# Optimization experiments

Hardware: AMD Instinct MI355X
Metric: run time of the kernel (lower is better)

## Reference

```python
import jax, jax.numpy as jnp
import numpy as np

N = 50000       # nodes
E = 800000      # edges (before self-loops)
IN = 64         # in_channels
OUT = 64        # out_channels


def setup_inputs() -> dict:
    key = jax.random.key(0)
    ks = jax.random.split(key, 6)
    X = jax.random.normal(ks[0], (N, IN), jnp.float32)
    H = jax.random.normal(ks[1], (N, OUT), jnp.float32)
    edge_index = jax.random.randint(ks[2], (2, E), 0, N, dtype=jnp.int64)
    edge_weight = jax.random.uniform(ks[3], (E,), jnp.float32)
    fan_in = IN + OUT
    W1 = jax.random.normal(ks[4], (fan_in, 2 * OUT), jnp.float32) / np.sqrt(fan_in).astype(np.float32)
    b1 = jnp.ones((2 * OUT,), jnp.float32)   # TGCN sets graph_conv1.bias to ones
    W2 = jax.random.normal(ks[5], (fan_in, OUT), jnp.float32) / np.sqrt(fan_in).astype(np.float32)
    b2 = jnp.zeros((OUT,), jnp.float32)      # default GCNConv bias init
    return {"X": X, "H": H, "edge_index": edge_index, "edge_weight": edge_weight,
            "W1": W1, "b1": b1, "W2": W2, "b2": b2}


def _gcn_conv(x, W, b, src, dst, w, n):
    """PyG GCNConv: linear transform, add self-loops (fill=1, improved=False),
    symmetric deg^-1/2 normalization, scatter-add aggregation at dst, + bias."""
    x = x @ W                                   # [N, out]
    loop = jnp.arange(n, dtype=src.dtype)
    s = jnp.concatenate([src, loop])            # [E+N]
    d = jnp.concatenate([dst, loop])
    ww = jnp.concatenate([w, jnp.ones((n,), x.dtype)])
    deg = jax.ops.segment_sum(ww, d, num_segments=n)
    dinv = jnp.where(deg > 0, jax.lax.rsqrt(jnp.maximum(deg, 1e-12)), 0.0)
    norm = dinv[s] * ww * dinv[d]               # [E+N]
    msg = x[s] * norm[:, None]                  # gather + scale
    out = jax.ops.segment_sum(msg, d, num_segments=n)  # scatter-add at dst
    return out + b


def reference(X, H, edge_index, edge_weight, W1, b1, W2, b2):
    src, dst = edge_index[0], edge_index[1]
    n = X.shape[0]
    ru = jax.nn.sigmoid(_gcn_conv(jnp.concatenate([X, H], axis=1), W1, b1, src, dst, edge_weight, n))
    r, u = ru[:, :OUT], ru[:, OUT:]             # chunk into reset/update gates
    c = jnp.tanh(_gcn_conv(jnp.concatenate([X, H * r], axis=1), W2, b2, src, dst, edge_weight, n))
    return u * H + (1.0 - u) * c                # new hidden state [N, OUT]
```

## Files before the change

### kernel.cpp

```cpp
#include <hip/hip_runtime.h>
#include <hip/hip_bf16.h>
#include <hip/hip_fp16.h>

#define NN 50000
#define NE 800000
#define NBIN ((NN + 255) / 256)
#define PB ((NE + 1023) / 1024)
#define GB ((NN + 63) / 64)
#define MAXB 4864

typedef __attribute__((ext_vector_type(8))) short bf16x8;
typedef __attribute__((ext_vector_type(4))) float f32x4;
typedef __attribute__((ext_vector_type(2))) float f32x2;

__device__ __forceinline__ unsigned int f2bf(float x) {
    unsigned int u = __float_as_uint(x);
    return (u + 0x7FFFu + ((u >> 16) & 1u)) >> 16;
}
__device__ __forceinline__ float bf2f(unsigned int b) {
    return __uint_as_float(b << 16);
}
__device__ __forceinline__ float4 f8x4_dec(unsigned int u) {
    f32x2 lo = __builtin_amdgcn_cvt_pk_f32_fp8(u, false);
    f32x2 hi = __builtin_amdgcn_cvt_pk_f32_fp8(u, true);
    float4 r; r.x = lo[0]; r.y = lo[1]; r.z = hi[0]; r.w = hi[1];
    return r;
}

__global__ void k_wprep(const float* __restrict__ W1, const float* __restrict__ W2,
                        unsigned short* __restrict__ Wf1,
                        unsigned short* __restrict__ Wf2t,
                        unsigned short* __restrict__ Wf2b) {
    int i = blockIdx.x * 256 + threadIdx.x;
    if (i < 16384) {
        int j = i & 7, l = (i >> 3) & 63, n = (i >> 9) & 7, kc = i >> 12;
        int k = kc * 32 + ((l >> 4) << 3) + j;
        int col = (n << 4) + (l & 15);
        Wf1[i] = (unsigned short)f2bf(W1[k * 128 + col]);
    }
    if (i < 4096) {
        int j = i & 7, l = (i >> 3) & 63, n = (i >> 9) & 3, kc = i >> 11;
        int k = kc * 32 + ((l >> 4) << 3) + j;
        int col = (n << 4) + (l & 15);
        Wf2t[i] = (unsigned short)f2bf(W2[k * 64 + col]);
        Wf2b[i] = (unsigned short)f2bf(W2[(k + 64) * 64 + col]);
    }
}

template <int OUTC, int KC, int SRC, int OMODE>
__device__ __forceinline__ void mgemm_core(
    const float* __restrict__ X, const float* __restrict__ Hm,
    const unsigned int* __restrict__ RUb, const unsigned short* __restrict__ Wf,
    const float* __restrict__ addF,
    unsigned short* __restrict__ outH, float* __restrict__ outF,
    unsigned char* __restrict__ outF8,
    int bid, unsigned short* aS, unsigned short* wS)
{
    constexpr int NT = OUTC / 16;
    const int tid = threadIdx.x;
    const int row0 = bid * 64;

    constexpr int WH = KC * NT * 64 * 8;
    {
        const uint4* Wg4 = reinterpret_cast<const uint4*>(Wf);
        uint4* wS4 = reinterpret_cast<uint4*>(wS);
        #pragma unroll
        for (int i = tid; i < WH / 8; i += 256) wS4[i] = Wg4[i];
    }
    #pragma unroll
    for (int i = tid; i < 64 * KC * 8; i += 256) {
        int row = i / (KC * 8), f4 = i % (KC * 8);
        int g = row0 + row;
        float4 v = {0.f, 0.f, 0.f, 0.f};
        if (g < NN) {
            if (SRC == 0) {
                v = (f4 < 16) ? reinterpret_cast<const float4*>(X)[g * 16 + f4]
                              : reinterpret_cast<const float4*>(Hm)[g * 16 + f4 - 16];
            } else if (SRC == 1) {
                v = reinterpret_cast<const float4*>(X)[g * 16 + f4];
            } else {
                v = reinterpret_cast<const float4*>(Hm)[g * 16 + f4];
                unsigned int r0 = RUb[g * 64 + 2 * f4];
                unsigned int r1 = RUb[g * 64 + 2 * f4 + 1];
                v.x *= bf2f(r0 & 0xFFFFu); v.y *= bf2f(r0 >> 16);
                v.z *= bf2f(r1 & 0xFFFFu); v.w *= bf2f(r1 >> 16);
            }
        }
        int k = f4 * 4;
        int kc = k >> 5, ko = k & 31;
        int l = (row & 15) | ((ko >> 3) << 4);
        int j0 = ko & 7;
        int m = row >> 4;
        uint2 pk;
        pk.x = f2bf(v.x) | (f2bf(v.y) << 16);
        pk.y = f2bf(v.z) | (f2bf(v.w) << 16);
        *reinterpret_cast<uint2*>(aS + (((m * KC + kc) * 64 + l) * 8 + j0)) = pk;
    }
    __syncthreads();

    const int wid = tid >> 6, l = tid & 63;
    f32x4 acc[NT];
    #pragma unroll
    for (int n = 0; n < NT; ++n) acc[n] = {0.f, 0.f, 0.f, 0.f};

    const bf16x8* aF = reinterpret_cast<const bf16x8*>(aS);
    const bf16x8* wF = reinterpret_cast<const bf16x8*>(wS);
    #pragma unroll
    for (int kc = 0; kc < KC; ++kc) {
        bf16x8 a = aF[(wid * KC + kc) * 64 + l];
        #pragma unroll
        for (int n = 0; n < NT; ++n) {
            bf16x8 b = wF[(kc * NT + n) * 64 + l];
            acc[n] = __builtin_amdgcn_mfma_f32_16x16x32_bf16(a, b, acc[n], 0, 0, 0);
        }
    }

    const int rbase = row0 + wid * 16 + ((l >> 4) << 2);
    const int cl = l & 15;
    #pragma unroll
    for (int n = 0; n < NT; ++n) {
        #pragma unroll
        for (int i = 0; i < 4; ++i) {
            int row = rbase + i;
            if (row >= NN) continue;
            int col = n * 16 + cl;
            if (OMODE == 1) {
                outF[(size_t)row * OUTC + col] = acc[n][i];
            } else if (OMODE == 2) {
                float a2 = acc[n][i] + addF[(size_t)row * OUTC + col];
                outH[(size_t)row * OUTC + col] = (unsigned short)f2bf(a2);
            } else {
                int q = __builtin_amdgcn_cvt_pk_fp8_f32(acc[n][i], acc[n][i], 0, false);
                outF8[(size_t)row * OUTC + col] = (unsigned char)(q & 0xFF);
            }
        }
    }
}

__launch_bounds__(256)
__global__ void k_build(const float* __restrict__ X, const float* __restrict__ Hm,
                        const unsigned short* __restrict__ Wf1,
                        const unsigned short* __restrict__ Wf2t,
                        unsigned char* __restrict__ Zf8, float* __restrict__ Z2p,
                        const int* __restrict__ dst, int* __restrict__ HT) {
    __shared__ unsigned short aS[8192];
    __shared__ unsigned short wS[16384];
    const int bid = blockIdx.x;
    const int tid = threadIdx.x;
    if (bid < PB) {
        int* hist = reinterpret_cast<int*>(aS);
        for (int i = tid; i < NBIN; i += 256) hist[i] = 0;
        __syncthreads();
        const int base = bid * 1024 + tid;
        #pragma unroll
        for (int k = 0; k < 4; ++k) {
            int e = base + k * 256;
            if (e < NE) atomicAdd(&hist[dst[e] >> 8], 1);
        }
        __syncthreads();
        for (int i = tid; i < NBIN; i += 256) HT[i * PB + bid] = hist[i];
        return;
    }
    if (bid < PB + GB) {
        mgemm_core<128, 4, 0, 3>(X, Hm, nullptr, Wf1, nullptr,
                                 nullptr, nullptr, Zf8, bid - PB, aS, wS);
        return;
    }
    mgemm_core<64, 2, 1, 1>(X, Hm, nullptr, Wf2t, nullptr,
                            nullptr, Z2p, nullptr, bid - PB - GB, aS, wS);
}

__launch_bounds__(256)
__global__ void k_gemm2b(const float* __restrict__ X, const float* __restrict__ Hm,
                         const unsigned int* __restrict__ RUb,
                         const unsigned short* __restrict__ Wf2b,
                         const float* __restrict__ Z2p,
                         unsigned short* __restrict__ Z2b) {
    __shared__ unsigned short aS[4096];
    __shared__ unsigned short wS[4096];
    mgemm_core<64, 2, 2, 2>(X, Hm, RUb, Wf2b, Z2p, Z2b, nullptr, nullptr,
                            blockIdx.x, aS, wS);
}

__launch_bounds__(256)
__global__ void k_scanA1(const int* __restrict__ HT, int* __restrict__ within,
                         int* __restrict__ binTot) {
    __shared__ int lds[PB];
    __shared__ int sc[256];
    __shared__ int carryS;
    const int b = blockIdx.x, tid = threadIdx.x;
    if (tid == 0) carryS = 0;
    for (int i = tid; i < PB; i += 256) lds[i] = HT[b * PB + i];
    __syncthreads();
    for (int c0 = 0; c0 < PB; c0 += 256) {
        int i = c0 + tid;
        int v = (i < PB) ? lds[i] : 0;
        sc[tid] = v;
        __syncthreads();
        #pragma unroll
        for (int off = 1; off < 256; off <<= 1) {
            int t = (tid >= off) ? sc[tid - off] : 0;
            __syncthreads();
            sc[tid] += t;
            __syncthreads();
        }
        int carry = carryS;
        if (i < PB) lds[i] = carry + sc[tid] - v;
        __syncthreads();
        if (tid == 255) carryS = carry + sc[255];
        __syncthreads();
    }
    for (int i = tid; i < PB; i += 256) within[b * PB + i] = lds[i];
    if (tid == 0) binTot[b] = carryS;
}

__launch_bounds__(256)
__global__ void k_scatterA(const int* __restrict__ src, const int* __restrict__ dst,
                           const float* __restrict__ w, const int* __restrict__ binTot,
                           const int* __restrict__ within, uint2* __restrict__ rec) {
    __shared__ int bS[256];
    __shared__ int cur[NBIN];
    const int blk = blockIdx.x, tid = threadIdx.x;
    int bv = (tid < NBIN) ? binTot[tid] : 0;
    bS[tid] = bv;
    __syncthreads();
    #pragma unroll
    for (int off = 1; off < 256; off <<= 1) {
        int t = (tid >= off) ? bS[tid - off] : 0;
        __syncthreads();
        bS[tid] += t;
        __syncthreads();
    }
    if (tid < NBIN) cur[tid] = (bS[tid] - bv) + within[tid * PB + blk];
    __syncthreads();
    const int base = blk * 1024 + tid;
    #pragma unroll
    for (int k = 0; k < 4; ++k) {
        int e = base + k * 256;
        if (e < NE) {
            int d = dst[e];
            int pos = atomicAdd(&cur[d >> 8], 1);
            unsigned int hn = __half_as_ushort(__float2half(w[e]));
            uint2 r;
            r.x = (unsigned int)src[e] | (hn << 16);
            r.y = (unsigned int)d;
            rec[pos] = r;
        }
    }
}

__launch_bounds__(256)
__global__ void k_phase2(const uint2* __restrict__ rec, const int* __restrict__ binTot,
                         unsigned int* __restrict__ snP, int* __restrict__ start,
                         float* __restrict__ dinv) {
    __shared__ unsigned int rSn[MAXB];
    __shared__ unsigned char rLo[MAXB];
    __shared__ unsigned int outSn[MAXB];
    __shared__ int cnt[256];
    __shared__ int sc[256];
    __shared__ int lstart[256];
    __shared__ int cur[256];
    const int b = blockIdx.x, tid = threadIdx.x;

    int bv = (tid < NBIN) ? binTot[tid] : 0;
    sc[tid] = bv;
    __syncthreads();
    #pragma unroll
    for (int off = 1; off < 256; off <<= 1) {
        int t = (tid >= off) ? sc[tid - off] : 0;
        __syncthreads();
        sc[tid] += t;
        __syncthreads();
    }
    const int e0 = (b == 0) ? 0 : sc[b - 1];
    int nE = sc[b] - e0;
    __syncthreads();
    if (nE > MAXB) nE = MAXB;

    cnt[tid] = 0;
    __syncthreads();
    for (int i = tid; i < nE; i += 256) {
        uint2 r = rec[e0 + i];
        rSn[i] = r.x;
        int lo = r.y & 255;
        rLo[i] = (unsigned char)lo;
        atomicAdd(&cnt[lo], 1);
    }
    __syncthreads();
    sc[tid] = cnt[tid];
    __syncthreads();
    #pragma unroll
    for (int off = 1; off < 256; off <<= 1) {
        int t = (tid >= off) ? sc[tid - off] : 0;
        __syncthreads();
        sc[tid] += t;
        __syncthreads();
    }
    lstart[tid] = sc[tid] - cnt[tid];
    cur[tid] = sc[tid] - cnt[tid];
    __syncthreads();
    const int node = b * 256 + tid;
    if (node <= NN) start[node] = e0 + lstart[tid];
    for (int i = tid; i < nE; i += 256) {
        int p = atomicAdd(&cur[rLo[i]], 1);
        outSn[p] = rSn[i];
    }
    __syncthreads();
    for (int i = tid; i < nE; i += 256) snP[e0 + i] = outSn[i];
    {
        int s0 = lstart[tid], c = cnt[tid];
        float sum = 0.f;
        for (int i = s0; i < s0 + c; ++i)
            sum += __half2float(__ushort_as_half((unsigned short)(outSn[i] >> 16)));
        if (node < NN) dinv[node] = rsqrtf(1.0f + sum);
    }
}

__launch_bounds__(256)
__global__ void k_gather1(const int* __restrict__ start, const unsigned int* __restrict__ snP,
                          const unsigned int* __restrict__ Zf8, const float* __restrict__ dinv,
                          const float* __restrict__ bias, uint2* __restrict__ RUb2) {
    const int node = blockIdx.x * 8 + (threadIdx.x >> 5);
    const int l = threadIdx.x & 31;
    if (node >= NN) return;

    const int e0 = start[node], e1 = start[node + 1];
    const float dvd = dinv[node];
    float4 acc = f8x4_dec(Zf8[(size_t)node * 32 + l]);
    acc.x *= dvd; acc.y *= dvd; acc.z *= dvd; acc.w *= dvd;

    #define EFMA8(U, NM) { float4 zz = f8x4_dec(U); \
        acc.x += zz.x * (NM); acc.y += zz.y * (NM); \
        acc.z += zz.z * (NM); acc.w += zz.w * (NM); }
    #define NMOF(SN) (dinv[(SN) & 0xFFFFu] * \
        __half2float(__ushort_as_half((unsigned short)((SN) >> 16))))

    int e = e0;
    for (; e + 8 <= e1; e += 8) {
        unsigned sn0 = snP[e],     sn1 = snP[e + 1], sn2 = snP[e + 2], sn3 = snP[e + 3];
        unsigned sn4 = snP[e + 4], sn5 = snP[e + 5], sn6 = snP[e + 6], sn7 = snP[e + 7];
        unsigned z0 = Zf8[(size_t)(sn0 & 0xFFFFu) * 32 + l];
        unsigned z1 = Zf8[(size_t)(sn1 & 0xFFFFu) * 32 + l];
        unsigned z2 = Zf8[(size_t)(sn2 & 0xFFFFu) * 32 + l];
        unsigned z3 = Zf8[(size_t)(sn3 & 0xFFFFu) * 32 + l];
        unsigned z4 = Zf8[(size_t)(sn4 & 0xFFFFu) * 32 + l];
        unsigned z5 = Zf8[(size_t)(sn5 & 0xFFFFu) * 32 + l];
        unsigned z6 = Zf8[(size_t)(sn6 & 0xFFFFu) * 32 + l];
        unsigned z7 = Zf8[(size_t)(sn7 & 0xFFFFu) * 32 + l];
        float n0 = NMOF(sn0), n1 = NMOF(sn1), n2 = NMOF(sn2), n3 = NMOF(sn3);
        float n4 = NMOF(sn4), n5 = NMOF(sn5), n6 = NMOF(sn6), n7 = NMOF(sn7);
        EFMA8(z0, n0) EFMA8(z1, n1) EFMA8(z2, n2) EFMA8(z3, n3)
        EFMA8(z4, n4) EFMA8(z5, n5) EFMA8(z6, n6) EFMA8(z7, n7)
    }
    if (e + 4 <= e1) {
        unsigned sn0 = snP[e], sn1 = snP[e + 1], sn2 = snP[e + 2], sn3 = snP[e + 3];
        unsigned z0 = Zf8[(size_t)(sn0 & 0xFFFFu) * 32 + l];
        unsigned z1 = Zf8[(size_t)(sn1 & 0xFFFFu) * 32 + l];
        unsigned z2 = Zf8[(size_t)(sn2 & 0xFFFFu) * 32 + l];
        unsigned z3 = Zf8[(size_t)(sn3 & 0xFFFFu) * 32 + l];
        float n0 = NMOF(sn0), n1 = NMOF(sn1), n2 = NMOF(sn2), n3 = NMOF(sn3);
        EFMA8(z0, n0) EFMA8(z1, n1) EFMA8(z2, n2) EFMA8(z3, n3)
        e += 4;
    }
    for (; e < e1; ++e) {
        unsigned sn = snP[e];
        unsigned z = Zf8[(size_t)(sn & 0xFFFFu) * 32 + l];
        float nm = NMOF(sn);
        EFMA8(z, nm)
    }
    #undef EFMA8
    #undef NMOF

    const int c = l * 4;
    float4 bb = *reinterpret_cast<const float4*>(bias + c);
    acc.x = acc.x * dvd + bb.x; acc.y = acc.y * dvd + bb.y;
    acc.z = acc.z * dvd + bb.z; acc.w = acc.w * dvd + bb.w;

    float4 o;
    o.x = 1.f / (1.f + expf(-acc.x));
    o.y = 1.f / (1.f + expf(-acc.y));
    o.z = 1.f / (1.f + expf(-acc.z));
    o.w = 1.f / (1.f + expf(-acc.w));
    uint2 pk;
    pk.x = f2bf(o.x) | (f2bf(o.y) << 16);
    pk.y = f2bf(o.z) | (f2bf(o.w) << 16);
    RUb2[(size_t)node * 32 + l] = pk;
}

__launch_bounds__(256)
__global__ void k_gather2(const int* __restrict__ start, const unsigned int* __restrict__ snP,
                          const uint2* __restrict__ Zb, const float* __restrict__ dinv,
                          const float* __restrict__ bias, const uint2* __restrict__ RUb2,
                          const float* __restrict__ Hm, float* __restrict__ out) {
    constexpr int GRP = 16;
    const int node = blockIdx.x * 16 + threadIdx.x / GRP;
    const int l = threadIdx.x % GRP;
    if (node >= NN) return;

    const int e0 = start[node], e1 = start[node + 1];
    const float dvd = dinv[node];

    uint2 zs = Zb[(size_t)node * GRP + l];
    float4 acc;
    acc.x = bf2f(zs.x & 0xFFFFu) * dvd;
    acc.y = bf2f(zs.x >> 16) * dvd;
    acc.z = bf2f(zs.y & 0xFFFFu) * dvd;
    acc.w = bf2f(zs.y >> 16) * dvd;

    #define EFMA(Z, NM) \
        acc.x += bf2f((Z).x & 0xFFFFu) * (NM); \
        acc.y += bf2f((Z).x >> 16) * (NM);     \
        acc.z += bf2f((Z).y & 0xFFFFu) * (NM); \
        acc.w += bf2f((Z).y >> 16) * (NM);
    #define NMOF(SN) (dinv[(SN) & 0xFFFFu] * \
        __half2float(__ushort_as_half((unsigned short)((SN) >> 16))))

    int e = e0;
    for (; e + 8 <= e1; e += 8) {
        unsigned sn0 = snP[e],     sn1 = snP[e + 1], sn2 = snP[e + 2], sn3 = snP[e + 3];
        unsigned sn4 = snP[e + 4], sn5 = snP[e + 5], sn6 = snP[e + 6], sn7 = snP[e + 7];
        uint2 z0 = Zb[(size_t)(sn0 & 0xFFFFu) * GRP + l];
        uint2 z1 = Zb[(size_t)(sn1 & 0xFFFFu) * GRP + l];
        uint2 z2 = Zb[(size_t)(sn2 & 0xFFFFu) * GRP + l];
        uint2 z3 = Zb[(size_t)(sn3 & 0xFFFFu) * GRP + l];
        uint2 z4 = Zb[(size_t)(sn4 & 0xFFFFu) * GRP + l];
        uint2 z5 = Zb[(size_t)(sn5 & 0xFFFFu) * GRP + l];
        uint2 z6 = Zb[(size_t)(sn6 & 0xFFFFu) * GRP + l];
        uint2 z7 = Zb[(size_t)(sn7 & 0xFFFFu) * GRP + l];
        float n0 = NMOF(sn0), n1 = NMOF(sn1), n2 = NMOF(sn2), n3 = NMOF(sn3);
        float n4 = NMOF(sn4), n5 = NMOF(sn5), n6 = NMOF(sn6), n7 = NMOF(sn7);
        EFMA(z0, n0) EFMA(z1, n1) EFMA(z2, n2) EFMA(z3, n3)
        EFMA(z4, n4) EFMA(z5, n5) EFMA(z6, n6) EFMA(z7, n7)
    }
    if (e + 4 <= e1) {
        unsigned sn0 = snP[e], sn1 = snP[e + 1], sn2 = snP[e + 2], sn3 = snP[e + 3];
        uint2 z0 = Zb[(size_t)(sn0 & 0xFFFFu) * GRP + l];
        uint2 z1 = Zb[(size_t)(sn1 & 0xFFFFu) * GRP + l];
        uint2 z2 = Zb[(size_t)(sn2 & 0xFFFFu) * GRP + l];
        uint2 z3 = Zb[(size_t)(sn3 & 0xFFFFu) * GRP + l];
        float n0 = NMOF(sn0), n1 = NMOF(sn1), n2 = NMOF(sn2), n3 = NMOF(sn3);
        EFMA(z0, n0) EFMA(z1, n1) EFMA(z2, n2) EFMA(z3, n3)
        e += 4;
    }
    for (; e < e1; ++e) {
        unsigned sn = snP[e];
        uint2 z = Zb[(size_t)(sn & 0xFFFFu) * GRP + l];
        float nm = NMOF(sn);
        EFMA(z, nm)
    }
    #undef EFMA
    #undef NMOF

    const int c = l * 4;
    float4 bb = *reinterpret_cast<const float4*>(bias + c);
    acc.x = acc.x * dvd + bb.x; acc.y = acc.y * dvd + bb.y;
    acc.z = acc.z * dvd + bb.z; acc.w = acc.w * dvd + bb.w;

    uint2 uu = RUb2[(size_t)node * 32 + 16 + l];
    float u0 = bf2f(uu.x & 0xFFFFu), u1 = bf2f(uu.x >> 16);
    float u2 = bf2f(uu.y & 0xFFFFu), u3 = bf2f(uu.y >> 16);
    float4 h4 = *reinterpret_cast<const float4*>(Hm + (size_t)node * 64 + c);
    float4 o;
    o.x = u0 * h4.x + (1.f - u0) * tanhf(acc.x);
    o.y = u1 * h4.y + (1.f - u1) * tanhf(acc.y);
    o.z = u2 * h4.z + (1.f - u2) * tanhf(acc.z);
    o.w = u3 * h4.w + (1.f - u3) * tanhf(acc.w);
    *reinterpret_cast<float4*>(out + (size_t)node * 64 + c) = o;
}

extern "C" void kernel_launch(void* const* d_in, const int* in_sizes, int n_in,
                              void* d_out, int out_size, void* d_ws, size_t ws_size,
                              hipStream_t stream) {
    const float* X  = (const float*)d_in[0];
    const float* Hm = (const float*)d_in[1];
    const int*   ei = (const int*)d_in[2];
    const float* w  = (const float*)d_in[3];
    const float* W1 = (const float*)d_in[4];
    const float* b1 = (const float*)d_in[5];
    const float* W2 = (const float*)d_in[6];
    const float* b2 = (const float*)d_in[7];
    float* out = (float*)d_out;

    const int* src = ei;
    const int* dst = ei + NE;

    char* p = (char*)d_ws;
    uint2* rec   = (uint2*)p;  p += sizeof(uint2) * NE;
    uint2* Z2b   = (uint2*)p;  p += sizeof(uint2) * NN * 16;
    uint2* RUb2  = (uint2*)p;  p += sizeof(uint2) * NN * 32;
    float* Z2p   = (float*)p;  p += sizeof(float) * NN * 64;
    float* dinv  = (float*)p;  p += sizeof(float) * NN;
    int*   start = (int*)p;    p += sizeof(int) * (NN + 1);
    int*   binTot   = (int*)p; p += sizeof(int) * (NBIN + 1);
    int*   HT       = (int*)p; p += sizeof(int) * NBIN * PB;
    int*   within   = (int*)p; p += sizeof(int) * NBIN * PB;
    unsigned int* snP = (unsigned int*)p; p += sizeof(unsigned int) * NE;
    unsigned int* Zf8 = (unsigned int*)p; p += sizeof(unsigned int) * NN * 32;
    unsigned short* Wf1  = (unsigned short*)p; p += sizeof(unsigned short) * 16384;
    unsigned short* Wf2t = (unsigned short*)p; p += sizeof(unsigned short) * 4096;
    unsigned short* Wf2b = (unsigned short*)p; p += sizeof(unsigned short) * 4096;

    k_wprep<<<64, 256, 0, stream>>>(W1, W2, Wf1, Wf2t, Wf2b);

    k_build<<<PB + 2 * GB, 256, 0, stream>>>(X, Hm, Wf1, Wf2t,
                                             (unsigned char*)Zf8, Z2p, dst, HT);

    k_scanA1<<<NBIN, 256, 0, stream>>>(HT, within, binTot);
    k_scatterA<<<PB, 256, 0, stream>>>(src, dst, w, binTot, within, rec);
    k_phase2<<<NBIN, 256, 0, stream>>>(rec, binTot, snP, start, dinv);

    k_gather1<<<(NN + 7) / 8, 256, 0, stream>>>(start, snP, Zf8, dinv, b1, RUb2);

    k_gemm2b<<<GB, 256, 0, stream>>>(X, Hm, (const unsigned int*)RUb2, Wf2b, Z2p,
                                     (unsigned short*)Z2b);
    k_gather2<<<(NN + 15) / 16, 256, 0, stream>>>(start, snP, Z2b, dinv, b2, RUb2, Hm, out);
}
```

Before: 114.7 us.

## Fuse reset-gated H·W2 GEMM into first gather kernel

Removes the separate k_gemm2b launch. The first gather kernel now computes (H*r)·W2_bottom per node with fp32 FMAs from LDS-resident weights, adds Z2p, and writes Z2b directly. It keeps only the update gate as bf16 for the second gather. This saves a launch and the round trip of the r gate through global memory. In exchange the gather becomes a persistent grid-stride kernel with block-wide syncs, LDS weights and scalar FMA instead of MFMA, which may reduce latency hiding in the gather.

```diff
diff --git a/kernel.cpp b/kernel.cpp
--- a/kernel.cpp
+++ b/kernel.cpp
@@ -29,8 +29,7 @@
 
 __global__ void k_wprep(const float* __restrict__ W1, const float* __restrict__ W2,
                         unsigned short* __restrict__ Wf1,
-                        unsigned short* __restrict__ Wf2t,
-                        unsigned short* __restrict__ Wf2b) {
+                        unsigned short* __restrict__ Wf2t) {
     int i = blockIdx.x * 256 + threadIdx.x;
     if (i < 16384) {
         int j = i & 7, l = (i >> 3) & 63, n = (i >> 9) & 7, kc = i >> 12;
@@ -43,17 +42,14 @@
         int k = kc * 32 + ((l >> 4) << 3) + j;
         int col = (n << 4) + (l & 15);
         Wf2t[i] = (unsigned short)f2bf(W2[k * 64 + col]);
-        Wf2b[i] = (unsigned short)f2bf(W2[(k + 64) * 64 + col]);
     }
 }
 
 template <int OUTC, int KC, int SRC, int OMODE>
 __device__ __forceinline__ void mgemm_core(
     const float* __restrict__ X, const float* __restrict__ Hm,
-    const unsigned int* __restrict__ RUb, const unsigned short* __restrict__ Wf,
-    const float* __restrict__ addF,
-    unsigned short* __restrict__ outH, float* __restrict__ outF,
-    unsigned char* __restrict__ outF8,
+    const unsigned short* __restrict__ Wf,
+    float* __restrict__ outF, unsigned char* __restrict__ outF8,
     int bid, unsigned short* aS, unsigned short* wS)
 {
     constexpr int NT = OUTC / 16;
@@ -76,14 +72,8 @@
             if (SRC == 0) {
                 v = (f4 < 16) ? reinterpret_cast<const float4*>(X)[g * 16 + f4]
                               : reinterpret_cast<const float4*>(Hm)[g * 16 + f4 - 16];
-            } else if (SRC == 1) {
+            } else {
                 v = reinterpret_cast<const float4*>(X)[g * 16 + f4];
-            } else {
-                v = reinterpret_cast<const float4*>(Hm)[g * 16 + f4];
-                unsigned int r0 = RUb[g * 64 + 2 * f4];
-                unsigned int r1 = RUb[g * 64 + 2 * f4 + 1];
-                v.x *= bf2f(r0 & 0xFFFFu); v.y *= bf2f(r0 >> 16);
-                v.z *= bf2f(r1 & 0xFFFFu); v.w *= bf2f(r1 >> 16);
             }
         }
         int k = f4 * 4;
@@ -126,9 +116,6 @@
             int col = n * 16 + cl;
             if (OMODE == 1) {
                 outF[(size_t)row * OUTC + col] = acc[n][i];
-            } else if (OMODE == 2) {
-                float a2 = acc[n][i] + addF[(size_t)row * OUTC + col];
-                outH[(size_t)row * OUTC + col] = (unsigned short)f2bf(a2);
             } else {
                 int q = __builtin_amdgcn_cvt_pk_fp8_f32(acc[n][i], acc[n][i], 0, false);
                 outF8[(size_t)row * OUTC + col] = (unsigned char)(q & 0xFF);
@@ -162,24 +149,10 @@
         return;
     }
     if (bid < PB + GB) {
-        mgemm_core<128, 4, 0, 3>(X, Hm, nullptr, Wf1, nullptr,
-                                 nullptr, nullptr, Zf8, bid - PB, aS, wS);
+        mgemm_core<128, 4, 0, 3>(X, Hm, Wf1, nullptr, Zf8, bid - PB, aS, wS);
         return;
     }
-    mgemm_core<64, 2, 1, 1>(X, Hm, nullptr, Wf2t, nullptr,
-                            nullptr, Z2p, nullptr, bid - PB - GB, aS, wS);
-}
-
-__launch_bounds__(256)
-__global__ void k_gemm2b(const float* __restrict__ X, const float* __restrict__ Hm,
-                         const unsigned int* __restrict__ RUb,
-                         const unsigned short* __restrict__ Wf2b,
-                         const float* __restrict__ Z2p,
-                         unsigned short* __restrict__ Z2b) {
-    __shared__ unsigned short aS[4096];
-    __shared__ unsigned short wS[4096];
-    mgemm_core<64, 2, 2, 2>(X, Hm, RUb, Wf2b, Z2p, Z2b, nullptr, nullptr,
-                            blockIdx.x, aS, wS);
+    mgemm_core<64, 2, 1, 1>(X, Hm, Wf2t, Z2p, nullptr, bid - PB - GB, aS, wS);
 }
 
 __launch_bounds__(256)
@@ -319,78 +292,117 @@
 __launch_bounds__(256)
 __global__ void k_gather1(const int* __restrict__ start, const unsigned int* __restrict__ snP,
                           const unsigned int* __restrict__ Zf8, const float* __restrict__ dinv,
-                          const float* __restrict__ bias, uint2* __restrict__ RUb2) {
-    const int node = blockIdx.x * 8 + (threadIdx.x >> 5);
-    const int l = threadIdx.x & 31;
-    if (node >= NN) return;
-
-    const int e0 = start[node], e1 = start[node + 1];
-    const float dvd = dinv[node];
-    float4 acc = f8x4_dec(Zf8[(size_t)node * 32 + l]);
-    acc.x *= dvd; acc.y *= dvd; acc.z *= dvd; acc.w *= dvd;
-
-    #define EFMA8(U, NM) { float4 zz = f8x4_dec(U); \
-        acc.x += zz.x * (NM); acc.y += zz.y * (NM); \
-        acc.z += zz.z * (NM); acc.w += zz.w * (NM); }
-    #define NMOF(SN) (dinv[(SN) & 0xFFFFu] * \
-        __half2float(__ushort_as_half((unsigned short)((SN) >> 16))))
-
-    int e = e0;
-    for (; e + 8 <= e1; e += 8) {
-        unsigned sn0 = snP[e],     sn1 = snP[e + 1], sn2 = snP[e + 2], sn3 = snP[e + 3];
-        unsigned sn4 = snP[e + 4], sn5 = snP[e + 5], sn6 = snP[e + 6], sn7 = snP[e + 7];
-        unsigned z0 = Zf8[(size_t)(sn0 & 0xFFFFu) * 32 + l];
-        unsigned z1 = Zf8[(size_t)(sn1 & 0xFFFFu) * 32 + l];
-        unsigned z2 = Zf8[(size_t)(sn2 & 0xFFFFu) * 32 + l];
-        unsigned z3 = Zf8[(size_t)(sn3 & 0xFFFFu) * 32 + l];
-        unsigned z4 = Zf8[(size_t)(sn4 & 0xFFFFu) * 32 + l];
-        unsigned z5 = Zf8[(size_t)(sn5 & 0xFFFFu) * 32 + l];
-        unsigned z6 = Zf8[(size_t)(sn6 & 0xFFFFu) * 32 + l];
-        unsigned z7 = Zf8[(size_t)(sn7 & 0xFFFFu) * 32 + l];
-        float n0 = NMOF(sn0), n1 = NMOF(sn1), n2 = NMOF(sn2), n3 = NMOF(sn3);
-        float n4 = NMOF(sn4), n5 = NMOF(sn5), n6 = NMOF(sn6), n7 = NMOF(sn7);
-        EFMA8(z0, n0) EFMA8(z1, n1) EFMA8(z2, n2) EFMA8(z3, n3)
-        EFMA8(z4, n4) EFMA8(z5, n5) EFMA8(z6, n6) EFMA8(z7, n7)
-    }
-    if (e + 4 <= e1) {
-        unsigned sn0 = snP[e], sn1 = snP[e + 1], sn2 = snP[e + 2], sn3 = snP[e + 3];
-        unsigned z0 = Zf8[(size_t)(sn0 & 0xFFFFu) * 32 + l];
-        unsigned z1 = Zf8[(size_t)(sn1 & 0xFFFFu) * 32 + l];
-        unsigned z2 = Zf8[(size_t)(sn2 & 0xFFFFu) * 32 + l];
-        unsigned z3 = Zf8[(size_t)(sn3 & 0xFFFFu) * 32 + l];
-        float n0 = NMOF(sn0), n1 = NMOF(sn1), n2 = NMOF(sn2), n3 = NMOF(sn3);
-        EFMA8(z0, n0) EFMA8(z1, n1) EFMA8(z2, n2) EFMA8(z3, n3)
-        e += 4;
-    }
-    for (; e < e1; ++e) {
-        unsigned sn = snP[e];
-        unsigned z = Zf8[(size_t)(sn & 0xFFFFu) * 32 + l];
-        float nm = NMOF(sn);
-        EFMA8(z, nm)
-    }
-    #undef EFMA8
-    #undef NMOF
-
-    const int c = l * 4;
-    float4 bb = *reinterpret_cast<const float4*>(bias + c);
-    acc.x = acc.x * dvd + bb.x; acc.y = acc.y * dvd + bb.y;
-    acc.z = acc.z * dvd + bb.z; acc.w = acc.w * dvd + bb.w;
-
-    float4 o;
-    o.x = 1.f / (1.f + expf(-acc.x));
-    o.y = 1.f / (1.f + expf(-acc.y));
-    o.z = 1.f / (1.f + expf(-acc.z));
-    o.w = 1.f / (1.f + expf(-acc.w));
-    uint2 pk;
-    pk.x = f2bf(o.x) | (f2bf(o.y) << 16);
-    pk.y = f2bf(o.z) | (f2bf(o.w) << 16);
-    RUb2[(size_t)node * 32 + l] = pk;
+                          const float* __restrict__ bias, const float* __restrict__ W2,
+                          const float* __restrict__ Z2p, const float* __restrict__ Hm,
+                          uint2* __restrict__ Ub, unsigned short* __restrict__ Z2b) {
+    __shared__ float wS[64 * 64];
+    __shared__ float hrS[8][64];
+    const int tid = threadIdx.x;
+    for (int i = tid; i < 4096; i += 256) wS[i] = W2[4096 + i];
+    __syncthreads();
+
+    const int nl = tid >> 5;
+    const int l = tid & 31;
+
+    for (int chunk = blockIdx.x; chunk * 8 < NN; chunk += gridDim.x) {
+        const int node = chunk * 8 + nl;
+        bool active = node < NN;
+        if (active) {
+            const int e0 = start[node], e1 = start[node + 1];
+            const float dvd = dinv[node];
+            float4 acc = f8x4_dec(Zf8[(size_t)node * 32 + l]);
+            acc.x *= dvd; acc.y *= dvd; acc.z *= dvd; acc.w *= dvd;
+
+            #define EFMA8(U, NM) { float4 zz = f8x4_dec(U); \
+                acc.x += zz.x * (NM); acc.y += zz.y * (NM); \
+                acc.z += zz.z * (NM); acc.w += zz.w * (NM); }
+            #define NMOF(SN) (dinv[(SN) & 0xFFFFu] * \
+                __half2float(__ushort_as_half((unsigned short)((SN) >> 16))))
+
+            int e = e0;
+            for (; e + 8 <= e1; e += 8) {
+                unsigned sn0 = snP[e],     sn1 = snP[e + 1], sn2 = snP[e + 2], sn3 = snP[e + 3];
+                unsigned sn4 = snP[e + 4], sn5 = snP[e + 5], sn6 = snP[e + 6], sn7 = snP[e + 7];
+                unsigned z0 = Zf8[(size_t)(sn0 & 0xFFFFu) * 32 + l];
+                unsigned z1 = Zf8[(size_t)(sn1 & 0xFFFFu) * 32 + l];
+                unsigned z2 = Zf8[(size_t)(sn2 & 0xFFFFu) * 32 + l];
+                unsigned z3 = Zf8[(size_t)(sn3 & 0xFFFFu) * 32 + l];
+                unsigned z4 = Zf8[(size_t)(sn4 & 0xFFFFu) * 32 + l];
+                unsigned z5 = Zf8[(size_t)(sn5 & 0xFFFFu) * 32 + l];
+                unsigned z6 = Zf8[(size_t)(sn6 & 0xFFFFu) * 32 + l];
+                unsigned z7 = Zf8[(size_t)(sn7 & 0xFFFFu) * 32 + l];
+                float n0 = NMOF(sn0), n1 = NMOF(sn1), n2 = NMOF(sn2), n3 = NMOF(sn3);
+                float n4 = NMOF(sn4), n5 = NMOF(sn5), n6 = NMOF(sn6), n7 = NMOF(sn7);
+                EFMA8(z0, n0) EFMA8(z1, n1) EFMA8(z2, n2) EFMA8(z3, n3)
+                EFMA8(z4, n4) EFMA8(z5, n5) EFMA8(z6, n6) EFMA8(z7, n7)
+            }
+            if (e + 4 <= e1) {
+                unsigned sn0 = snP[e], sn1 = snP[e + 1], sn2 = snP[e + 2], sn3 = snP[e + 3];
+                unsigned z0 = Zf8[(size_t)(sn0 & 0xFFFFu) * 32 + l];
+                unsigned z1 = Zf8[(size_t)(sn1 & 0xFFFFu) * 32 + l];
+                unsigned z2 = Zf8[(size_t)(sn2 & 0xFFFFu) * 32 + l];
+                unsigned z3 = Zf8[(size_t)(sn3 & 0xFFFFu) * 32 + l];
+                float n0 = NMOF(sn0), n1 = NMOF(sn1), n2 = NMOF(sn2), n3 = NMOF(sn3);
+                EFMA8(z0, n0) EFMA8(z1, n1) EFMA8(z2, n2) EFMA8(z3, n3)
+                e += 4;
+            }
+            for (; e < e1; ++e) {
+                unsigned sn = snP[e];
+                unsigned z = Zf8[(size_t)(sn & 0xFFFFu) * 32 + l];
+                float nm = NMOF(sn);
+                EFMA8(z, nm)
+            }
+            #undef EFMA8
+            #undef NMOF
+
+            const int c = l * 4;
+            float4 bb = *reinterpret_cast<const float4*>(bias + c);
+            acc.x = acc.x * dvd + bb.x; acc.y = acc.y * dvd + bb.y;
+            acc.z = acc.z * dvd + bb.z; acc.w = acc.w * dvd + bb.w;
+
+            float4 o;
+            o.x = 1.f / (1.f + expf(-acc.x));
+            o.y = 1.f / (1.f + expf(-acc.y));
+            o.z = 1.f / (1.f + expf(-acc.z));
+            o.w = 1.f / (1.f + expf(-acc.w));
+
+            if (l >= 16) {
+                uint2 pk;
+                pk.x = f2bf(o.x) | (f2bf(o.y) << 16);
+                pk.y = f2bf(o.z) | (f2bf(o.w) << 16);
+                Ub[(size_t)node * 16 + (l - 16)] = pk;
+            } else {
+                float4 h4 = *reinterpret_cast<const float4*>(Hm + (size_t)node * 64 + c);
+                hrS[nl][c + 0] = o.x * h4.x;
+                hrS[nl][c + 1] = o.y * h4.y;
+                hrS[nl][c + 2] = o.z * h4.z;
+                hrS[nl][c + 3] = o.w * h4.w;
+            }
+        }
+        __syncthreads();
+        if (active) {
+            const int c0 = l * 2;
+            float a0 = 0.f, a1 = 0.f;
+            #pragma unroll 8
+            for (int k = 0; k < 64; ++k) {
+                float hv = hrS[nl][k];
+                a0 += hv * wS[k * 64 + c0];
+                a1 += hv * wS[k * 64 + c0 + 1];
+            }
+            float2 zp = *reinterpret_cast<const float2*>(Z2p + (size_t)node * 64 + c0);
+            ushort2 st;
+            st.x = (unsigned short)f2bf(a0 + zp.x);
+            st.y = (unsigned short)f2bf(a1 + zp.y);
+            *reinterpret_cast<ushort2*>(Z2b + (size_t)node * 64 + c0) = st;
+        }
+        __syncthreads();
+    }
 }
 
 __launch_bounds__(256)
 __global__ void k_gather2(const int* __restrict__ start, const unsigned int* __restrict__ snP,
                           const uint2* __restrict__ Zb, const float* __restrict__ dinv,
-                          const float* __restrict__ bias, const uint2* __restrict__ RUb2,
+                          const float* __restrict__ bias, const uint2* __restrict__ Ub,
                           const float* __restrict__ Hm, float* __restrict__ out) {
     constexpr int GRP = 16;
     const int node = blockIdx.x * 16 + threadIdx.x / GRP;
@@ -456,7 +468,7 @@
     acc.x = acc.x * dvd + bb.x; acc.y = acc.y * dvd + bb.y;
     acc.z = acc.z * dvd + bb.z; acc.w = acc.w * dvd + bb.w;
 
-    uint2 uu = RUb2[(size_t)node * 32 + 16 + l];
+    uint2 uu = Ub[(size_t)node * 16 + l];
     float u0 = bf2f(uu.x & 0xFFFFu), u1 = bf2f(uu.x >> 16);
     float u2 = bf2f(uu.y & 0xFFFFu), u3 = bf2f(uu.y >> 16);
     float4 h4 = *reinterpret_cast<const float4*>(Hm + (size_t)node * 64 + c);
@@ -487,7 +499,7 @@
     char* p = (char*)d_ws;
     uint2* rec   = (uint2*)p;  p += sizeof(uint2) * NE;
     uint2* Z2b   = (uint2*)p;  p += sizeof(uint2) * NN * 16;
-    uint2* RUb2  = (uint2*)p;  p += sizeof(uint2) * NN * 32;
+    uint2* Ub    = (uint2*)p;  p += sizeof(uint2) * NN * 16;
     float* Z2p   = (float*)p;  p += sizeof(float) * NN * 64;
     float* dinv  = (float*)p;  p += sizeof(float) * NN;
     int*   start = (int*)p;    p += sizeof(int) * (NN + 1);
@@ -498,9 +510,8 @@
     unsigned int* Zf8 = (unsigned int*)p; p += sizeof(unsigned int) * NN * 32;
     unsigned short* Wf1  = (unsigned short*)p; p += sizeof(unsigned short) * 16384;
     unsigned short* Wf2t = (unsigned short*)p; p += sizeof(unsigned short) * 4096;
-    unsigned short* Wf2b = (unsigned short*)p; p += sizeof(unsigned short) * 4096;
-
-    k_wprep<<<64, 256, 0, stream>>>(W1, W2, Wf1, Wf2t, Wf2b);
+
+    k_wprep<<<64, 256, 0, stream>>>(W1, W2, Wf1, Wf2t);
 
     k_build<<<PB + 2 * GB, 256, 0, stream>>>(X, Hm, Wf1, Wf2t,
                                              (unsigned char*)Zf8, Z2p, dst, HT);
@@ -509,9 +520,8 @@
     k_scatterA<<<PB, 256, 0, stream>>>(src, dst, w, binTot, within, rec);
     k_phase2<<<NBIN, 256, 0, stream>>>(rec, binTot, snP, start, dinv);
 
-    k_gather1<<<(NN + 7) / 8, 256, 0, stream>>>(start, snP, Zf8, dinv, b1, RUb2);
-
-    k_gemm2b<<<GB, 256, 0, stream>>>(X, Hm, (const unsigned int*)RUb2, Wf2b, Z2p,
-                                     (unsigned short*)Z2b);
-    k_gather2<<<(NN + 15) / 16, 256, 0, stream>>>(start, snP, Z2b, dinv, b2, RUb2, Hm, out);
-}
+    k_gather1<<<1024, 256, 0, stream>>>(start, snP, Zf8, dinv, b1, W2, Z2p, Hm, Ub,
+                                        (unsigned short*)Z2b);
+
+    k_gather2<<<(NN + 15) / 16, 256, 0, stream>>>(start, snP, Z2b, dinv, b2, Ub, Hm, out);
+}
```

Measured after the change: 127.4 us. 1.11x slower.
